# Kernel tuning notes

Hardware: AMD Instinct MI355X
Metric: run time of the kernel (lower is better)

## Reference

```python
import jax, jax.numpy as jnp
import numpy as np

INPUT_SIZE = (224, 224)


def setup_inputs() -> dict:
    key = jax.random.key(0)
    k1, k2, k3 = jax.random.split(key, 3)
    feat2 = jax.random.normal(k1, (16, 512, 28, 28), dtype=jnp.float32)
    feat3 = jax.random.normal(k2, (16, 1024, 14, 14), dtype=jnp.float32)
    memory_bank = jax.random.normal(k3, (16384, 1536), dtype=jnp.float32)
    return {"feat2": feat2, "feat3": feat3, "memory_bank": memory_bank}


def reference(feat2, feat3, memory_bank):
    b, c2, h, w = feat2.shape
    c3 = feat3.shape[1]
    # interpolate(feat3, size=(h,w), mode='bilinear', align_corners=False)
    feat3_up = jax.image.resize(feat3, (b, c3, h, w), method='bilinear')
    features = jnp.concatenate([feat2, feat3_up], axis=1)  # [b, c, h, w]
    c = c2 + c3
    feats = features.transpose(0, 2, 3, 1).reshape(-1, c)  # [N, c]
    x_sq = jnp.sum(feats * feats, axis=1, keepdims=True)            # [N, 1]
    m_sq = jnp.sum(memory_bank * memory_bank, axis=1)[None, :]      # [1, M]
    d2 = x_sq + m_sq - 2.0 * (feats @ memory_bank.T)                # [N, M]
    min_d = jnp.sqrt(jnp.maximum(jnp.min(d2, axis=1), 0.0))         # [N]
    anomaly_map = min_d.reshape(b, 1, h, w)
    anomaly_map = jax.image.resize(
        anomaly_map, (b, 1, INPUT_SIZE[0], INPUT_SIZE[1]), method='bilinear')
    pred_score = jnp.max(anomaly_map.reshape(b, -1), axis=1)
    return anomaly_map, pred_score
```

## Files before the change

### kernel.cpp

```cpp
#include <hip/hip_runtime.h>
#include <math.h>

#define N_ROWS 12544
#define C_DIM  1536
#define M_ROWS 16384
#define BATCH  16

#define QS    16.0f
#define S2x2  0.0078125f
#define S2    0.00390625f

typedef int   i32x4 __attribute__((ext_vector_type(4)));
typedef unsigned char u8;
typedef signed char   i8;

__device__ __forceinline__ unsigned fkey(float f) {
  unsigned u = __float_as_uint(f);
  return (u & 0x80000000u) ? ~u : (u | 0x80000000u);
}
__device__ __forceinline__ float funkey(unsigned k) {
  unsigned u = (k & 0x80000000u) ? (k ^ 0x80000000u) : ~k;
  return __uint_as_float(u);
}

__device__ __forceinline__ void gl_lds16(const void* g, void* l) {
  __builtin_amdgcn_global_load_lds(
      (__attribute__((address_space(1))) void*)(g),
      (__attribute__((address_space(3))) void*)(l), 16, 0, 0);
}

__device__ __forceinline__ int quant(float v) {
  int q = __float2int_rn(v * QS);
  return max(-127, min(127, q));
}

__global__ void prep_all(const float* __restrict__ feat2,
                         const float* __restrict__ feat3,
                         const float* __restrict__ mb,
                         i8* __restrict__ feats, i8* __restrict__ mbb,
                         float* __restrict__ xsq, float* __restrict__ msq,
                         unsigned* __restrict__ dmin,
                         unsigned* __restrict__ score) {
  const int blk = blockIdx.x;
  const int t = threadIdx.x;
  __shared__ float sred[4];

  if (blk < M_ROWS) {
    const int j = blk;
    const float* in = mb + (size_t)j * C_DIM;
    i8* outp = mbb + (size_t)j * C_DIM;
    float ssq = 0.f;
    {
      const float4 v = *(const float4*)(in + t * 4);
      int q0 = quant(v.x), q1 = quant(v.y), q2 = quant(v.z), q3 = quant(v.w);
      unsigned w = (unsigned)(q0 & 0xFF) | ((unsigned)(q1 & 0xFF) << 8)
                 | ((unsigned)(q2 & 0xFF) << 16) | ((unsigned)(q3 & 0xFF) << 24);
      *(unsigned*)(outp + t * 4) = w;
      ssq = (float)(q0*q0 + q1*q1 + q2*q2 + q3*q3);
    }
    if (t < 128) {
      const int i2 = 256 + t;
      const float4 v = *(const float4*)(in + i2 * 4);
      int q0 = quant(v.x), q1 = quant(v.y), q2 = quant(v.z), q3 = quant(v.w);
      unsigned w = (unsigned)(q0 & 0xFF) | ((unsigned)(q1 & 0xFF) << 8)
                 | ((unsigned)(q2 & 0xFF) << 16) | ((unsigned)(q3 & 0xFF) << 24);
      *(unsigned*)(outp + i2 * 4) = w;
      ssq += (float)(q0*q0 + q1*q1 + q2*q2 + q3*q3);
    }
    for (int off = 32; off > 0; off >>= 1) ssq += __shfl_down(ssq, off, 64);
    if ((t & 63) == 0) sred[t >> 6] = ssq;
    __syncthreads();
    if (t == 0) msq[j] = S2 * (sred[0] + sred[1] + sred[2] + sred[3]);
  } else {
    const int n = blk - M_ROWS;
    const int b = n / 784;
    const int rem = n % 784;
    const int y = rem / 28, x = rem % 28;
    const float sy = 0.5f * y - 0.25f;
    const float sx = 0.5f * x - 0.25f;
    const int y0 = (int)floorf(sy); const float fy = sy - (float)y0;
    const int x0 = (int)floorf(sx); const float fx = sx - (float)x0;
    const int y0c = max(y0, 0), y1c = min(y0 + 1, 13);
    const int x0c = max(x0, 0), x1c = min(x0 + 1, 13);
    const float w00 = (1.f-fy)*(1.f-fx), w01 = (1.f-fy)*fx;
    const float w10 = fy*(1.f-fx),       w11 = fy*fx;

    float ssq = 0.f;
    i8* orow = feats + (size_t)n * C_DIM;
    for (int c = t; c < C_DIM; c += 256) {
      float v;
      if (c < 512) {
        v = feat2[(((size_t)b * 512 + c) * 28 + y) * 28 + x];
      } else {
        const float* f3 = feat3 + ((size_t)b * 1024 + (c - 512)) * 196;
        v = w00 * f3[y0c*14 + x0c] + w01 * f3[y0c*14 + x1c]
          + w10 * f3[y1c*14 + x0c] + w11 * f3[y1c*14 + x1c];
      }
      int q = quant(v);
      orow[c] = (i8)q;
      ssq += (float)(q * q);
    }
    for (int off = 32; off > 0; off >>= 1) ssq += __shfl_down(ssq, off, 64);
    if ((t & 63) == 0) sred[t >> 6] = ssq;
    __syncthreads();
    if (t == 0) {
      xsq[n] = S2 * (sred[0] + sred[1] + sred[2] + sred[3]);
      dmin[n] = 0xFFFFFFFFu;
    }
    if (n == 0 && t < BATCH) score[t] = 0u;
  }
}

__global__ void gemm_min(const i8* __restrict__ X, const i8* __restrict__ Mb,
                         const float* __restrict__ msq,
                         unsigned* __restrict__ dmin) {
  __shared__ u8 As[16384];
  __shared__ u8 Bs[16384];
  __shared__ unsigned smin[128];
  const int t = threadIdx.x;
  const int mtile = blockIdx.x;
  const int ntile = blockIdx.y;
  const int lane = t & 63, wave = t >> 6;
  const int wm = wave >> 1, wn = wave & 1;
  if (t < 128) smin[t] = 0xFFFFFFFFu;

  const int row0 = ntile * 128;
  const int col0 = mtile * 128;
  const int s_row = t >> 2;
  const int s_ch  = (t & 3) ^ ((t >> 3) & 3);
  const i8* ga = X  + (size_t)(row0 + s_row) * C_DIM + s_ch * 16;
  const i8* gb = Mb + (size_t)(col0 + s_row) * C_DIM + s_ch * 16;
  u8* la = As + t * 16;
  u8* lb = Bs + t * 16;

  i32x4 acc[4][4];
  const i32x4 zero = {0, 0, 0, 0};
#pragma unroll
  for (int mi = 0; mi < 4; mi++)
#pragma unroll
    for (int ni = 0; ni < 4; ni++) acc[mi][ni] = zero;

  const int quad = lane >> 4, l16 = lane & 15;
  const int fsw = (l16 >> 1) & 3;
  const int slot = ((quad ^ fsw) * 16);
  const u8* arow = As + (wm * 64 + l16) * 64 + slot;
  const u8* brow = Bs + (wn * 64 + l16) * 64 + slot;

  for (int k0 = 0; k0 < C_DIM; k0 += 128) {
    __syncthreads();
    gl_lds16(ga + k0,                    la);
    gl_lds16(ga + 64 * C_DIM + k0,       la + 4096);
    gl_lds16(ga + k0 + 64,               la + 8192);
    gl_lds16(ga + 64 * C_DIM + k0 + 64,  la + 12288);
    gl_lds16(gb + k0,                    lb);
    gl_lds16(gb + 64 * C_DIM + k0,       lb + 4096);
    gl_lds16(gb + k0 + 64,               lb + 8192);
    gl_lds16(gb + 64 * C_DIM + k0 + 64,  lb + 12288);
    __syncthreads();
#pragma unroll
    for (int sub = 0; sub < 2; sub++) {
      i32x4 af[4], bf[4];
#pragma unroll
      for (int mi = 0; mi < 4; mi++)
        af[mi] = *(const i32x4*)(arow + sub * 8192 + mi * 1024);
#pragma unroll
      for (int ni = 0; ni < 4; ni++)
        bf[ni] = *(const i32x4*)(brow + sub * 8192 + ni * 1024);
#pragma unroll
      for (int mi = 0; mi < 4; mi++)
#pragma unroll
        for (int ni = 0; ni < 4; ni++)
          acc[mi][ni] = __builtin_amdgcn_mfma_i32_16x16x64_i8(
              af[mi], bf[ni], acc[mi][ni], 0, 0, 0);
    }
  }

  float msql[4];
#pragma unroll
  for (int ni = 0; ni < 4; ni++)
    msql[ni] = msq[col0 + wn * 64 + ni * 16 + l16];

#pragma unroll
  for (int mi = 0; mi < 4; mi++) {
#pragma unroll
    for (int r = 0; r < 4; r++) {
      float v = msql[0] - S2x2 * (float)acc[mi][0][r];
#pragma unroll
      for (int ni = 1; ni < 4; ni++)
        v = fminf(v, msql[ni] - S2x2 * (float)acc[mi][ni][r]);
      v = fminf(v, __shfl_xor(v, 1, 64));
      v = fminf(v, __shfl_xor(v, 2, 64));
      v = fminf(v, __shfl_xor(v, 4, 64));
      v = fminf(v, __shfl_xor(v, 8, 64));
      if (l16 == 0) {
        int lrow = wm * 64 + mi * 16 + quad * 4 + r;
        atomicMin(&smin[lrow], fkey(v));
      }
    }
  }
  __syncthreads();
  if (t < 128) atomicMin(&dmin[row0 + t], smin[t]);
}

__global__ void finalize(const unsigned* __restrict__ dmin,
                         const float* __restrict__ xsq,
                         float* __restrict__ out) {
  const int b = blockIdx.x, slice = blockIdx.y, t = threadIdx.x;
  __shared__ float smap[784];
  __shared__ float sred[4];
  for (int i = t; i < 784; i += 256) {
    float d2 = xsq[b * 784 + i] + funkey(dmin[b * 784 + i]);
    smap[i] = sqrtf(fmaxf(d2, 0.f));
  }
  __syncthreads();
  float* omap = out + (size_t)b * 50176;
  float tmax = 0.f;
  const int p0 = slice * 6272;
  for (int p = p0 + t; p < p0 + 6272; p += 256) {
    const int Y = p / 224, Xp = p % 224;
    const float sy = Y * 0.125f - 0.4375f;
    const float sx = Xp * 0.125f - 0.4375f;
    const int y0 = (int)floorf(sy); const float fy = sy - (float)y0;
    const int x0 = (int)floorf(sx); const float fx = sx - (float)x0;
    const int y0c = max(y0, 0), y1c = min(y0 + 1, 27);
    const int x0c = max(x0, 0), x1c = min(x0 + 1, 27);
    float v = (1.f-fy)*((1.f-fx)*smap[y0c*28+x0c] + fx*smap[y0c*28+x1c])
            +      fy *((1.f-fx)*smap[y1c*28+x0c] + fx*smap[y1c*28+x1c]);
    omap[p] = v;
    tmax = fmaxf(tmax, v);
  }
  for (int off = 32; off > 0; off >>= 1)
    tmax = fmaxf(tmax, __shfl_down(tmax, off, 64));
  if ((t & 63) == 0) sred[t >> 6] = tmax;
  __syncthreads();
  if (t == 0) {
    float m = fmaxf(fmaxf(sred[0], sred[1]), fmaxf(sred[2], sred[3]));
    atomicMax((unsigned*)(out + 802816 + b), __float_as_uint(m));
  }
}

extern "C" void kernel_launch(void* const* d_in, const int* in_sizes, int n_in,
                              void* d_out, int out_size, void* d_ws, size_t ws_size,
                              hipStream_t stream) {
  const float* feat2 = (const float*)d_in[0];
  const float* feat3 = (const float*)d_in[1];
  const float* mb    = (const float*)d_in[2];
  char* ws = (char*)d_ws;
  i8*       feats = (i8*)ws;
  i8*       mbb   = (i8*)(ws + 19267584);
  float*    xsq   = (float*)(ws + 44433408);
  float*    msq   = (float*)(ws + 44483584);
  unsigned* dmin  = (unsigned*)(ws + 44549120);
  float* out = (float*)d_out;

  prep_all<<<M_ROWS + N_ROWS, 256, 0, stream>>>(
      feat2, feat3, mb, feats, mbb, xsq, msq, dmin,
      (unsigned*)(out + 802816));
  gemm_min<<<dim3(128, 98), 256, 0, stream>>>(feats, mbb, msq, dmin);
  finalize<<<dim3(BATCH, 8), 256, 0, stream>>>(dmin, xsq, out);
}
```

Baseline: 594.9 us.

## Enlarge GEMM tile to 256x256 with double-buffered LDS prefetch pipeline

The int8 GEMM-min kernel grows from 128x128 tiles with 4 waves to 256x256 tiles with 8 waves, each wave holding 8x4 MFMA accumulators. Global-to-LDS loads are double-buffered and issued in phases interleaved with MFMA work, using explicit vmcnt waits, raw barriers and s_setprio to overlap memory with compute. The aim is more data reuse per byte loaded and hidden load latency. The cost is higher register and LDS pressure, with 128KB of LDS per block, and fewer blocks, which can lower occupancy and leave the wave tail less balanced.

```diff
diff --git a/kernel.cpp b/kernel.cpp
--- a/kernel.cpp
+++ b/kernel.cpp
@@ -111,69 +111,119 @@
   }
 }
 
-__global__ void gemm_min(const i8* __restrict__ X, const i8* __restrict__ Mb,
-                         const float* __restrict__ msq,
-                         unsigned* __restrict__ dmin) {
-  __shared__ u8 As[16384];
-  __shared__ u8 Bs[16384];
-  __shared__ unsigned smin[128];
+__global__ __launch_bounds__(512, 2) void gemm_min(
+    const i8* __restrict__ X, const i8* __restrict__ Mb,
+    const float* __restrict__ msq, unsigned* __restrict__ dmin) {
+  __shared__ u8 sA[65536];
+  __shared__ u8 sB[65536];
+  __shared__ unsigned smin[256];
+
   const int t = threadIdx.x;
+  const int lane = t & 63, wave = t >> 6;
+  const int wm = wave >> 2, wn = wave & 3;
+  const int quad = lane >> 4, l16 = lane & 15;
+  const int fsw = (l16 >> 1) & 3;
   const int mtile = blockIdx.x;
   const int ntile = blockIdx.y;
-  const int lane = t & 63, wave = t >> 6;
-  const int wm = wave >> 1, wn = wave & 1;
-  if (t < 128) smin[t] = 0xFFFFFFFFu;
-
-  const int row0 = ntile * 128;
-  const int col0 = mtile * 128;
-  const int s_row = t >> 2;
-  const int s_ch  = (t & 3) ^ ((t >> 3) & 3);
-  const i8* ga = X  + (size_t)(row0 + s_row) * C_DIM + s_ch * 16;
-  const i8* gb = Mb + (size_t)(col0 + s_row) * C_DIM + s_ch * 16;
-  u8* la = As + t * 16;
-  u8* lb = Bs + t * 16;
-
-  i32x4 acc[4][4];
+  const int row0 = ntile * 256;
+  const int col0 = mtile * 256;
+
+  if (t < 256) smin[t] = 0xFFFFFFFFu;
+
+  const int srow = t >> 2;
+  const int sch  = (t & 3) ^ ((t >> 3) & 3);
+  const i8* gA = X  + (size_t)(row0 + srow) * C_DIM + sch * 16;
+  const i8* gB = Mb + (size_t)(col0 + srow) * C_DIM + sch * 16;
+  u8* lA = sA + t * 16;
+  u8* lB = sB + t * 16;
+
+  const int aoff = (wm * 128 + l16) * 64 + (quad ^ fsw) * 16;
+  const int boff = (wn * 64  + l16) * 64 + (quad ^ fsw) * 16;
+
+  i32x4 acc[8][4];
   const i32x4 zero = {0, 0, 0, 0};
 #pragma unroll
-  for (int mi = 0; mi < 4; mi++)
+  for (int mi = 0; mi < 8; mi++)
 #pragma unroll
     for (int ni = 0; ni < 4; ni++) acc[mi][ni] = zero;
 
-  const int quad = lane >> 4, l16 = lane & 15;
-  const int fsw = (l16 >> 1) & 3;
-  const int slot = ((quad ^ fsw) * 16);
-  const u8* arow = As + (wm * 64 + l16) * 64 + slot;
-  const u8* brow = Bs + (wn * 64 + l16) * 64 + slot;
-
-  for (int k0 = 0; k0 < C_DIM; k0 += 128) {
-    __syncthreads();
-    gl_lds16(ga + k0,                    la);
-    gl_lds16(ga + 64 * C_DIM + k0,       la + 4096);
-    gl_lds16(ga + k0 + 64,               la + 8192);
-    gl_lds16(ga + 64 * C_DIM + k0 + 64,  la + 12288);
-    gl_lds16(gb + k0,                    lb);
-    gl_lds16(gb + 64 * C_DIM + k0,       lb + 4096);
-    gl_lds16(gb + k0 + 64,               lb + 8192);
-    gl_lds16(gb + 64 * C_DIM + k0 + 64,  lb + 12288);
-    __syncthreads();
-#pragma unroll
-    for (int sub = 0; sub < 2; sub++) {
-      i32x4 af[4], bf[4];
-#pragma unroll
-      for (int mi = 0; mi < 4; mi++)
-        af[mi] = *(const i32x4*)(arow + sub * 8192 + mi * 1024);
-#pragma unroll
-      for (int ni = 0; ni < 4; ni++)
-        bf[ni] = *(const i32x4*)(brow + sub * 8192 + ni * 1024);
-#pragma unroll
-      for (int mi = 0; mi < 4; mi++)
-#pragma unroll
-        for (int ni = 0; ni < 4; ni++)
-          acc[mi][ni] = __builtin_amdgcn_mfma_i32_16x16x64_i8(
-              af[mi], bf[ni], acc[mi][ni], 0, 0, 0);
-    }
-  }
+  i32x4 af[4], bf[4];
+
+#define STAGE_A(KT, S) { \
+    const i8* g_ = gA + (KT) * 128 + (S) * 64; \
+    u8* l_ = lA + ((KT) & 1) * 32768 + (S) * 16384; \
+    gl_lds16(g_, l_); gl_lds16(g_ + (size_t)128 * C_DIM, l_ + 8192); }
+#define STAGE_B(KT, S) { \
+    const i8* g_ = gB + (KT) * 128 + (S) * 64; \
+    u8* l_ = lB + ((KT) & 1) * 32768 + (S) * 16384; \
+    gl_lds16(g_, l_); gl_lds16(g_ + (size_t)128 * C_DIM, l_ + 8192); }
+#define WAIT_VM(N) asm volatile("s_waitcnt vmcnt(" #N ")" ::: "memory")
+#define MFMA16(Q) \
+    _Pragma("unroll") \
+    for (int mi = 0; mi < 4; mi++) { \
+      _Pragma("unroll") \
+      for (int ni = 0; ni < 4; ni++) \
+        acc[(Q)*4+mi][ni] = __builtin_amdgcn_mfma_i32_16x16x64_i8( \
+            af[mi], bf[ni], acc[(Q)*4+mi][ni], 0, 0, 0); }
+#define PHASE0(S, STAGE, TAIL) { \
+    const u8* ab_ = sA + cur * 32768 + (S) * 16384 + aoff; \
+    af[0] = *(const i32x4*)(ab_); \
+    af[1] = *(const i32x4*)(ab_ + 1024); \
+    af[2] = *(const i32x4*)(ab_ + 2048); \
+    af[3] = *(const i32x4*)(ab_ + 3072); \
+    const u8* bb_ = sB + cur * 32768 + (S) * 16384 + boff; \
+    bf[0] = *(const i32x4*)(bb_); \
+    bf[1] = *(const i32x4*)(bb_ + 1024); \
+    bf[2] = *(const i32x4*)(bb_ + 2048); \
+    bf[3] = *(const i32x4*)(bb_ + 3072); \
+    STAGE; \
+    __builtin_amdgcn_s_barrier(); \
+    asm volatile("s_waitcnt lgkmcnt(0)" ::: "memory"); \
+    __builtin_amdgcn_s_setprio(1); MFMA16(0); __builtin_amdgcn_s_setprio(0); \
+    TAIL; \
+    __builtin_amdgcn_s_barrier(); }
+#define PHASE1(S, STAGE, TAIL) { \
+    const u8* ab_ = sA + cur * 32768 + (S) * 16384 + aoff; \
+    af[0] = *(const i32x4*)(ab_ + 4096); \
+    af[1] = *(const i32x4*)(ab_ + 5120); \
+    af[2] = *(const i32x4*)(ab_ + 6144); \
+    af[3] = *(const i32x4*)(ab_ + 7168); \
+    STAGE; \
+    __builtin_amdgcn_s_barrier(); \
+    asm volatile("s_waitcnt lgkmcnt(0)" ::: "memory"); \
+    __builtin_amdgcn_s_setprio(1); MFMA16(1); __builtin_amdgcn_s_setprio(0); \
+    TAIL; \
+    __builtin_amdgcn_s_barrier(); }
+
+  STAGE_A(0, 0); STAGE_B(0, 0); STAGE_A(0, 1); STAGE_B(0, 1);
+  STAGE_A(1, 0); STAGE_B(1, 0);
+  WAIT_VM(8);
+  __builtin_amdgcn_s_barrier();
+
+  int cur = 0;
+  for (int kt = 0; kt < 10; ++kt) {
+    PHASE0(0, STAGE_A(kt + 1, 1), );
+    PHASE1(0, STAGE_B(kt + 1, 1), WAIT_VM(8));
+    PHASE0(1, STAGE_A(kt + 2, 0), );
+    PHASE1(1, STAGE_B(kt + 2, 0), WAIT_VM(8));
+    cur ^= 1;
+  }
+  PHASE0(0, STAGE_A(11, 1), );
+  PHASE1(0, STAGE_B(11, 1), WAIT_VM(8));
+  PHASE0(1, , );
+  PHASE1(1, , WAIT_VM(4));
+  cur ^= 1;
+  PHASE0(0, , );
+  PHASE1(0, , WAIT_VM(0));
+  PHASE0(1, , );
+  PHASE1(1, , );
+
+#undef PHASE1
+#undef PHASE0
+#undef MFMA16
+#undef WAIT_VM
+#undef STAGE_B
+#undef STAGE_A
 
   float msql[4];
 #pragma unroll
@@ -181,25 +231,24 @@
     msql[ni] = msq[col0 + wn * 64 + ni * 16 + l16];
 
 #pragma unroll
-  for (int mi = 0; mi < 4; mi++) {
+  for (int mi8 = 0; mi8 < 8; mi8++) {
 #pragma unroll
     for (int r = 0; r < 4; r++) {
-      float v = msql[0] - S2x2 * (float)acc[mi][0][r];
+      float v = msql[0] - S2x2 * (float)acc[mi8][0][r];
 #pragma unroll
       for (int ni = 1; ni < 4; ni++)
-        v = fminf(v, msql[ni] - S2x2 * (float)acc[mi][ni][r]);
+        v = fminf(v, msql[ni] - S2x2 * (float)acc[mi8][ni][r]);
       v = fminf(v, __shfl_xor(v, 1, 64));
       v = fminf(v, __shfl_xor(v, 2, 64));
       v = fminf(v, __shfl_xor(v, 4, 64));
       v = fminf(v, __shfl_xor(v, 8, 64));
       if (l16 == 0) {
-        int lrow = wm * 64 + mi * 16 + quad * 4 + r;
-        atomicMin(&smin[lrow], fkey(v));
+        atomicMin(&smin[wm * 128 + mi8 * 16 + quad * 4 + r], fkey(v));
       }
     }
   }
   __syncthreads();
-  if (t < 128) atomicMin(&dmin[row0 + t], smin[t]);
+  if (t < 256) atomicMin(&dmin[row0 + t], smin[t]);
 }
 
 __global__ void finalize(const unsigned* __restrict__ dmin,
@@ -256,6 +305,6 @@
   prep_all<<<M_ROWS + N_ROWS, 256, 0, stream>>>(
       feat2, feat3, mb, feats, mbb, xsq, msq, dmin,
       (unsigned*)(out + 802816));
-  gemm_min<<<dim3(128, 98), 256, 0, stream>>>(feats, mbb, msq, dmin);
+  gemm_min<<<dim3(64, 49), 512, 0, stream>>>(feats, mbb, msq, dmin);
   finalize<<<dim3(BATCH, 8), 256, 0, stream>>>(dmin, xsq, out);
 }
```

Measured after the change: 696.8 us. 1.17x slower.

## Restructure feature prep to process image rows with LDS staging and coalesced loads

Applied to the files above, without the earlier changes.

The feature-prep path now assigns one block per (batch, image row) instead of one block per pixel. Lanes read feat2 and feat3 coalesced along x, compute the bilinear upsample with wave shuffles, quantize into an LDS tile, and then write 16-byte vectors to global memory, accumulating row norms with LDS atomics. The aim is to remove the strided, uncoalesced per-channel gathers of the old per-pixel layout. The memory-bank blocks now run with 512 threads, and 128 of them sit idle. The 28*1552-byte LDS array is declared for every block, including the bank-quantization blocks, which may lower their occupancy.

```diff
diff --git a/kernel.cpp b/kernel.cpp
--- a/kernel.cpp
+++ b/kernel.cpp
@@ -34,23 +34,26 @@
   return max(-127, min(127, q));
 }
 
-__global__ void prep_all(const float* __restrict__ feat2,
-                         const float* __restrict__ feat3,
-                         const float* __restrict__ mb,
-                         i8* __restrict__ feats, i8* __restrict__ mbb,
-                         float* __restrict__ xsq, float* __restrict__ msq,
-                         unsigned* __restrict__ dmin,
-                         unsigned* __restrict__ score) {
+#define FSTRIDE 1552
+
+__global__ __launch_bounds__(512) void prep_all(
+    const float* __restrict__ feat2, const float* __restrict__ feat3,
+    const float* __restrict__ mb,
+    i8* __restrict__ feats, i8* __restrict__ mbb,
+    float* __restrict__ xsq, float* __restrict__ msq,
+    unsigned* __restrict__ dmin, unsigned* __restrict__ score) {
   const int blk = blockIdx.x;
   const int t = threadIdx.x;
-  __shared__ float sred[4];
+  __shared__ float sred[8];
+  __shared__ u8 fsm[28 * FSTRIDE];
+  __shared__ int sxq[28];
 
   if (blk < M_ROWS) {
     const int j = blk;
     const float* in = mb + (size_t)j * C_DIM;
     i8* outp = mbb + (size_t)j * C_DIM;
     float ssq = 0.f;
-    {
+    if (t < 384) {
       const float4 v = *(const float4*)(in + t * 4);
       int q0 = quant(v.x), q1 = quant(v.y), q2 = quant(v.z), q3 = quant(v.w);
       unsigned w = (unsigned)(q0 & 0xFF) | ((unsigned)(q1 & 0xFF) << 8)
@@ -58,56 +61,82 @@
       *(unsigned*)(outp + t * 4) = w;
       ssq = (float)(q0*q0 + q1*q1 + q2*q2 + q3*q3);
     }
-    if (t < 128) {
-      const int i2 = 256 + t;
-      const float4 v = *(const float4*)(in + i2 * 4);
-      int q0 = quant(v.x), q1 = quant(v.y), q2 = quant(v.z), q3 = quant(v.w);
-      unsigned w = (unsigned)(q0 & 0xFF) | ((unsigned)(q1 & 0xFF) << 8)
-                 | ((unsigned)(q2 & 0xFF) << 16) | ((unsigned)(q3 & 0xFF) << 24);
-      *(unsigned*)(outp + i2 * 4) = w;
-      ssq += (float)(q0*q0 + q1*q1 + q2*q2 + q3*q3);
-    }
     for (int off = 32; off > 0; off >>= 1) ssq += __shfl_down(ssq, off, 64);
     if ((t & 63) == 0) sred[t >> 6] = ssq;
     __syncthreads();
-    if (t == 0) msq[j] = S2 * (sred[0] + sred[1] + sred[2] + sred[3]);
+    if (t == 0) {
+      float s = 0.f;
+#pragma unroll
+      for (int wv = 0; wv < 6; wv++) s += sred[wv];
+      msq[j] = S2 * s;
+    }
+    if (blk == 0 && t < BATCH) score[t] = 0u;
   } else {
-    const int n = blk - M_ROWS;
-    const int b = n / 784;
-    const int rem = n % 784;
-    const int y = rem / 28, x = rem % 28;
+    const int f = blk - M_ROWS;
+    const int b = f / 28, y = f % 28;
+    const int n0 = b * 784 + y * 28;
+
     const float sy = 0.5f * y - 0.25f;
-    const float sx = 0.5f * x - 0.25f;
     const int y0 = (int)floorf(sy); const float fy = sy - (float)y0;
+    const int y0c = max(y0, 0), y1c = min(y0 + 1, 13);
+    const float wy0 = 1.f - fy, wy1 = fy;
+
+    const int g  = t >> 5;
+    const int l2 = t & 31;
+    const float sx = 0.5f * l2 - 0.25f;
     const int x0 = (int)floorf(sx); const float fx = sx - (float)x0;
-    const int y0c = max(y0, 0), y1c = min(y0 + 1, 13);
     const int x0c = max(x0, 0), x1c = min(x0 + 1, 13);
-    const float w00 = (1.f-fy)*(1.f-fx), w01 = (1.f-fy)*fx;
-    const float w10 = fy*(1.f-fx),       w11 = fy*fx;
-
-    float ssq = 0.f;
-    i8* orow = feats + (size_t)n * C_DIM;
-    for (int c = t; c < C_DIM; c += 256) {
-      float v;
-      if (c < 512) {
-        v = feat2[(((size_t)b * 512 + c) * 28 + y) * 28 + x];
-      } else {
-        const float* f3 = feat3 + ((size_t)b * 1024 + (c - 512)) * 196;
-        v = w00 * f3[y0c*14 + x0c] + w01 * f3[y0c*14 + x1c]
-          + w10 * f3[y1c*14 + x0c] + w11 * f3[y1c*14 + x1c];
-      }
-      int q = quant(v);
-      orow[c] = (i8)q;
-      ssq += (float)(q * q);
-    }
-    for (int off = 32; off > 0; off >>= 1) ssq += __shfl_down(ssq, off, 64);
-    if ((t & 63) == 0) sred[t >> 6] = ssq;
-    __syncthreads();
-    if (t == 0) {
-      xsq[n] = S2 * (sred[0] + sred[1] + sred[2] + sred[3]);
-      dmin[n] = 0xFFFFFFFFu;
-    }
-    if (n == 0 && t < BATCH) score[t] = 0u;
+    const float wx0 = 1.f - fx, wx1 = fx;
+
+    if (t < 28) sxq[t] = 0;
+
+    const float* f2b = feat2 + (size_t)b * 512 * 784 + y * 28;
+#pragma unroll 4
+    for (int i = 0; i < 32; i++) {
+      const int c = i * 16 + g;
+      if (l2 < 28) {
+        float v = f2b[(size_t)c * 784 + l2];
+        fsm[l2 * FSTRIDE + c] = (u8)(i8)quant(v);
+      }
+    }
+
+    const float* f3b = feat3 + (size_t)b * 1024 * 196;
+#pragma unroll 4
+    for (int i = 0; i < 64; i++) {
+      const int cc = i * 16 + g;
+      const float* f3 = f3b + (size_t)cc * 196;
+      float v = 0.f;
+      if (l2 < 14)       v = f3[y0c * 14 + l2];
+      else if (l2 < 28)  v = f3[y1c * 14 + (l2 - 14)];
+      float t0 = wy0 * __shfl(v, x0c, 32)      + wy1 * __shfl(v, 14 + x0c, 32);
+      float t1 = wy0 * __shfl(v, x1c, 32)      + wy1 * __shfl(v, 14 + x1c, 32);
+      if (l2 < 28) {
+        float o = wx0 * t0 + wx1 * t1;
+        fsm[l2 * FSTRIDE + 512 + cc] = (u8)(i8)quant(o);
+      }
+    }
+    __syncthreads();
+
+    i8* orow = feats + (size_t)n0 * C_DIM;
+    for (int idx = t; idx < 28 * 96; idx += 512) {
+      const int row = idx / 96, col = idx % 96;
+      i32x4 wv = *(const i32x4*)(fsm + row * FSTRIDE + col * 16);
+      *(i32x4*)(orow + (size_t)row * C_DIM + col * 16) = wv;
+      int s = 0;
+#pragma unroll
+      for (int k = 0; k < 4; k++) {
+        const int w = wv[k];
+        const int b0 = (int)(i8)(w & 0xFF), b1 = (int)(i8)((w >> 8) & 0xFF);
+        const int b2 = (int)(i8)((w >> 16) & 0xFF), b3 = (int)(i8)(w >> 24);
+        s += b0*b0 + b1*b1 + b2*b2 + b3*b3;
+      }
+      atomicAdd(&sxq[row], s);
+    }
+    __syncthreads();
+    if (t < 28) {
+      xsq[n0 + t] = S2 * (float)sxq[t];
+      dmin[n0 + t] = 0xFFFFFFFFu;
+    }
   }
 }
 
@@ -253,7 +282,7 @@
   unsigned* dmin  = (unsigned*)(ws + 44549120);
   float* out = (float*)d_out;
 
-  prep_all<<<M_ROWS + N_ROWS, 256, 0, stream>>>(
+  prep_all<<<M_ROWS + 448, 512, 0, stream>>>(
       feat2, feat3, mb, feats, mbb, xsq, msq, dmin,
       (unsigned*)(out + 802816));
   gemm_min<<<dim3(128, 98), 256, 0, stream>>>(feats, mbb, msq, dmin);
```

Result: faster. 532.1 us (-10.6%).
